# Kernel optimization log

Measured on AMD Instinct MI355X. Metric: run time of the kernel, lower is better.

## Reference

```python
import jax, jax.numpy as jnp
import numpy as np

N_NODES = 50000
N_EDGES = 600000
D = 128

def _linear_params(key, fan_in, fan_out):
    # torch nn.Linear default init: U(-1/sqrt(fan_in), 1/sqrt(fan_in))
    k1, k2 = jax.random.split(key)
    bound = 1.0 / np.sqrt(fan_in)
    W = jax.random.uniform(k1, (fan_in, fan_out), minval=-bound, maxval=bound, dtype=jnp.float32)
    b = jax.random.uniform(k2, (fan_out,), minval=-bound, maxval=bound, dtype=jnp.float32)
    return W, b

def setup_inputs() -> dict:
    key = jax.random.key(0)
    kh, ke, k1, k2, k3, k4 = jax.random.split(key, 6)
    h = jax.random.normal(kh, (N_NODES, D), dtype=jnp.float32)
    edges = jax.random.randint(ke, (N_EDGES, 2), 0, N_NODES, dtype=jnp.int32)
    msg_W1, msg_b1 = _linear_params(k1, 2 * D, D)
    msg_W2, msg_b2 = _linear_params(k2, D, D)
    upd_W1, upd_b1 = _linear_params(k3, 2 * D, D)
    upd_W2, upd_b2 = _linear_params(k4, D, D)
    return {"h": h, "edges": edges,
            "msg_W1": msg_W1, "msg_b1": msg_b1, "msg_W2": msg_W2, "msg_b2": msg_b2,
            "upd_W1": upd_W1, "upd_b1": upd_b1, "upd_W2": upd_W2, "upd_b2": upd_b2}

def reference(h, edges, msg_W1, msg_b1, msg_W2, msg_b2, upd_W1, upd_b1, upd_W2, upd_b2):
    src = edges[:, 0]
    dst = edges[:, 1]
    # message MLP over concatenated [h_src, h_dst] per edge: [E, 2D] -> [E, D]
    pair = jnp.concatenate([h[src], h[dst]], axis=-1)
    msg = jax.nn.relu(pair @ msg_W1 + msg_b1) @ msg_W2 + msg_b2
    # scatter-add aggregate messages onto destination nodes: [N, D]
    agg = jax.ops.segment_sum(msg, dst, num_segments=h.shape[0])
    # update MLP on [h, agg]: [N, 2D] -> [N, D]
    upd_in = jnp.concatenate([h, agg], axis=-1)
    h_new = jax.nn.relu(upd_in @ upd_W1 + upd_b1) @ upd_W2 + upd_b2
    return h + h_new
```

## Files before the change

kernel.cpp:

```cpp
#include <hip/hip_runtime.h>
#include <hip/hip_bf16.h>

#define NN 50000
#define NE 600000
#define TN 64
#define NT ((NN + TN - 1) / TN)
#define CAP 1024

typedef unsigned short u16;
typedef unsigned int u32;
typedef unsigned long long u64;
typedef __attribute__((ext_vector_type(8))) short bf16x8;
typedef __attribute__((ext_vector_type(16))) float f32x16;
typedef __attribute__((ext_vector_type(4))) int int4v;

#define SM_AB   0
#define SM_TT   16384
#define SM_ST   32768
#define SM_S    40960
#define SM_BIAS 49152
#define SMEM_TOTAL 50176

__device__ __forceinline__ void bar_lds() {
    asm volatile("s_waitcnt lgkmcnt(0)" ::: "memory");
    __builtin_amdgcn_s_barrier();
}

__device__ __forceinline__ u16 f2b(float x) {
    __hip_bfloat16 b = __float2bfloat16(x);
    union { __hip_bfloat16 b; u16 u; } c; c.b = b; return c.u;
}
__device__ __forceinline__ int4v zero4() {
    int4v v; v[0]=0; v[1]=0; v[2]=0; v[3]=0; return v;
}
__device__ __forceinline__ f32x16 zero16() {
    f32x16 z;
#pragma unroll
    for (int i = 0; i < 16; ++i) z[i] = 0.f;
    return z;
}
__device__ __forceinline__ int4v cvt8(const float* __restrict__ p) {
    const float4* q = (const float4*)p;
    float4 f0 = q[0], f1 = q[1];
    union { u16 u[8]; int4v v; } r;
    r.u[0]=f2b(f0.x); r.u[1]=f2b(f0.y); r.u[2]=f2b(f0.z); r.u[3]=f2b(f0.w);
    r.u[4]=f2b(f1.x); r.u[5]=f2b(f1.y); r.u[6]=f2b(f1.z); r.u[7]=f2b(f1.w);
    return r.v;
}
__device__ __forceinline__ u64 pack4(float a, float b, float c, float d) {
    union { u16 u[4]; u64 q; } r;
    r.u[0]=f2b(a); r.u[1]=f2b(b); r.u[2]=f2b(c); r.u[3]=f2b(d); return r.q;
}
__device__ __forceinline__ f32x16 mfma16(bf16x8 a, bf16x8 b, f32x16 c) {
    return __builtin_amdgcn_mfma_f32_32x32x16_bf16(a, b, c, 0, 0, 0);
}
__device__ __forceinline__ bf16x8 ld256(const char* base, int row, int c) {
    return *(const bf16x8*)(base + row * 256 + ((c ^ (row & 15)) << 4));
}
__device__ __forceinline__ bf16x8 ld128r(const char* base, int row, int c) {
    return *(const bf16x8*)(base + row * 128 + ((c ^ (row & 7)) << 4));
}

__global__ void prep_kernel(const float* __restrict__ h,
                            const float* __restrict__ W1m, const float* __restrict__ W2m,
                            const float* __restrict__ W1u, const float* __restrict__ W2u,
                            u16* __restrict__ w1tm, u16* __restrict__ w2tm,
                            u16* __restrict__ w1tu, u16* __restrict__ w2tu,
                            u16* __restrict__ hbuf, int do_h)
{
    int tid = blockIdx.x * blockDim.x + threadIdx.x;
    int stride = gridDim.x * blockDim.x;
    for (int i = tid; i < 128 * 256; i += stride) {
        int n = i >> 8, k = i & 255;
        w1tm[i] = f2b(W1m[k * 128 + n]);
        w1tu[i] = f2b(W1u[k * 128 + n]);
    }
    for (int i = tid; i < 128 * 128; i += stride) {
        int n = i >> 7, k = i & 127;
        w2tm[i] = f2b(W2m[k * 128 + n]);
        w2tu[i] = f2b(W2u[k * 128 + n]);
    }
    if (do_h) {
        for (int i = tid; i < NN * 128 / 8; i += stride)
            *(int4v*)(hbuf + (size_t)i * 8) = cvt8(h + (size_t)i * 8);
    }
}

__global__ __launch_bounds__(256) void scatter_kernel(
    const int* __restrict__ edges, u32* __restrict__ elist, int* __restrict__ cursor)
{
    __shared__ int lcnt[NT];
    const int e0 = blockIdx.x * 2048;
    for (int i = threadIdx.x; i < NT; i += 256) lcnt[i] = 0;
    __syncthreads();
#pragma unroll
    for (int k = 0; k < 8; ++k) {
        int e = e0 + k * 256 + threadIdx.x;
        if (e < NE) atomicAdd(&lcnt[edges[2 * e + 1] >> 6], 1);
    }
    __syncthreads();
    for (int i = threadIdx.x; i < NT; i += 256) {
        int cn = lcnt[i];
        if (cn > 0) lcnt[i] = atomicAdd(&cursor[i], cn);
    }
    __syncthreads();
#pragma unroll
    for (int k = 0; k < 8; ++k) {
        int e = e0 + k * 256 + threadIdx.x;
        if (e < NE) {
            int s = edges[2 * e], d = edges[2 * e + 1];
            int bin = d >> 6;
            int pos = atomicAdd(&lcnt[bin], 1);
            if (pos < CAP) elist[(size_t)bin * CAP + pos] = (u32)s | ((u32)(d & 63) << 16);
        }
    }
}

__global__ __launch_bounds__(256, 2) void fused_kernel(
    const float* __restrict__ h, const u16* __restrict__ hb, int use_hb,
    const u32* __restrict__ elist, const int* __restrict__ cursor,
    const u16* __restrict__ w1m, const u16* __restrict__ w2m,
    const u16* __restrict__ w1u, const u16* __restrict__ w2u,
    const float* __restrict__ b1m, const float* __restrict__ b2m,
    const float* __restrict__ b1u, const float* __restrict__ b2u,
    float* __restrict__ outp)
{
    extern __shared__ char sm[];
    char* ab   = sm + SM_AB;
    char* ttr  = sm + SM_TT;
    char* Stb  = sm + SM_ST;
    char* Sb   = sm + SM_S;
    char* bias = sm + SM_BIAS;
    char* htu  = sm + SM_ST;

    const int tid  = threadIdx.x;
    const int lane = tid & 63;
    const int wid  = tid >> 6;
    const int l31  = lane & 31;
    const int kg   = lane >> 5;
    const int nrow  = wid * 32 + l31;
    const int ecol0 = l31;
    const int ecol1 = 32 + l31;

    const int bin = blockIdx.x;
    const int n0  = bin * TN;
    int size = cursor[bin]; if (size > CAP) size = CAP;
    const u32* el = elist + (size_t)bin * CAP;
    const int nchunk = (size + 63) >> 6;

    bf16x8 w1f[8], w2f[8];
#pragma unroll
    for (int kk = 0; kk < 8; ++kk) {
        w1f[kk] = *(const bf16x8*)(w1m + nrow * 256 + (kk * 2 + kg) * 8);
        w2f[kk] = *(const bf16x8*)(w2m + nrow * 128 + (kk * 2 + kg) * 8);
    }
    const float b2ms = b2m[nrow];

    for (int i = tid; i < 1024; i += 256) {
        int row = i >> 4, c = i & 15;
        int node = n0 + row;
        int4v v = zero4();
        if (node < NN) {
            if (use_hb) v = *(const int4v*)(hb + (size_t)node * 128 + c * 8);
            else        v = cvt8(h + (size_t)node * 128 + c * 8);
        }
        *(int4v*)(ttr + row * 256 + ((c ^ (row & 15)) << 4)) = v;
    }
    if (tid < 32)      *(float4*)(bias + tid * 16)          = ((const float4*)b1m)[tid];
    else if (tid < 64) *(float4*)(bias + 512 + (tid-32)*16) = ((const float4*)b1u)[tid - 32];
    {
        char* z = sm + SM_ST + tid * 64;
        *(int4v*)z = zero4(); *(int4v*)(z + 16) = zero4();
        *(int4v*)(z + 32) = zero4(); *(int4v*)(z + 48) = zero4();
    }

    auto put_St = [&](u32 rec, int cb2, u16 val) {
        if (cb2 + lane < size) {
            int d = (int)((rec >> 16) & 63);
            *(u16*)(Stb + lane * 128 + (((d >> 3) ^ (lane & 7)) << 4) + (d & 7) * 2) = val;
        }
    };
    auto put_S = [&](u32 rec, int cb2, u16 val) {
        if (cb2 + lane < size) {
            int d = (int)((rec >> 16) & 63);
            *(u16*)(Sb + d * 128 + (((lane >> 3) ^ (d & 7)) << 4) + (lane & 7) * 2) = val;
        }
    };

    const int s_row0 = tid >> 4, s_cc = tid & 15;
    auto stage_load = [&](u32 dle_c, int cb2, int4v* v) {
#pragma unroll
        for (int u = 0; u < 4; ++u) {
            int row = s_row0 + 16 * u;
            int s = ((int)__shfl((int)dle_c, row, 64)) & 0xFFFF;
            v[u] = zero4();
            if (cb2 + row < size)
                v[u] = use_hb ? *(const int4v*)(hb + (size_t)s * 128 + s_cc * 8)
                              : cvt8(h + (size_t)s * 128 + s_cc * 8);
        }
    };
    auto stage_write = [&](const int4v* v) {
#pragma unroll
        for (int u = 0; u < 4; ++u) {
            int row = s_row0 + 16 * u;
            *(int4v*)(ab + row * 256 + ((s_cc ^ (row & 15)) << 4)) = v[u];
        }
    };

    auto mkfrags = [&](const f32x16& cc, bf16x8& lo, bf16x8& hi) {
        u32 u0,u1,u2,u3,u4,u5,u6,u7;
        {
            float a0=cc[0]+b2ms, a1=cc[1]+b2ms, a2=cc[2]+b2ms, a3=cc[3]+b2ms;
            float a4=cc[4]+b2ms, a5=cc[5]+b2ms, a6=cc[6]+b2ms, a7=cc[7]+b2ms;
            float a8=cc[8]+b2ms, a9=cc[9]+b2ms, aA=cc[10]+b2ms, aB=cc[11]+b2ms;
            float aC=cc[12]+b2ms, aD=cc[13]+b2ms, aE=cc[14]+b2ms, aF=cc[15]+b2ms;
            asm("v_cvt_pk_bf16_f32 %0, %1, %2" : "=v"(u0) : "v"(a0), "v"(a1));
            asm("v_cvt_pk_bf16_f32 %0, %1, %2" : "=v"(u1) : "v"(a2), "v"(a3));
            asm("v_cvt_pk_bf16_f32 %0, %1, %2" : "=v"(u2) : "v"(a4), "v"(a5));
            asm("v_cvt_pk_bf16_f32 %0, %1, %2" : "=v"(u3) : "v"(a6), "v"(a7));
            asm("v_cvt_pk_bf16_f32 %0, %1, %2" : "=v"(u4) : "v"(a8), "v"(a9));
            asm("v_cvt_pk_bf16_f32 %0, %1, %2" : "=v"(u5) : "v"(aA), "v"(aB));
            asm("v_cvt_pk_bf16_f32 %0, %1, %2" : "=v"(u6) : "v"(aC), "v"(aD));
            asm("v_cvt_pk_bf16_f32 %0, %1, %2" : "=v"(u7) : "v"(aE), "v"(aF));
        }
        asm volatile("v_permlane32_swap_b32 %0, %1" : "+v"(u0), "+v"(u2));
        asm volatile("v_permlane32_swap_b32 %0, %1" : "+v"(u1), "+v"(u3));
        asm volatile("v_permlane32_swap_b32 %0, %1" : "+v"(u4), "+v"(u6));
        asm volatile("v_permlane32_swap_b32 %0, %1" : "+v"(u5), "+v"(u7));
        union { u32 w[4]; bf16x8 v; } A, B;
        A.w[0]=u0; A.w[1]=u1; A.w[2]=u2; A.w[3]=u3;
        B.w[0]=u4; B.w[1]=u5; B.w[2]=u6; B.w[3]=u7;
        lo = A.v; hi = B.v;
    };

    u32 dle = (lane < size) ? el[lane] : 0u;
    if (nchunk > 0) {
        int4v v[4];
        stage_load(dle, 0, v);
        stage_write(v);
    }
    __syncthreads();

    f32x16 t0 = zero16(), t1 = zero16();
    {
        __builtin_amdgcn_s_setprio(1);
#pragma unroll
        for (int kk = 0; kk < 8; ++kk) {
            bf16x8 wtf = *(const bf16x8*)(w1m + nrow * 256 + (16 + kk * 2 + kg) * 8);
            int ch = kk * 2 + kg;
            t0 = mfma16(wtf, ld256(ttr, ecol0, ch), t0);
            t1 = mfma16(wtf, ld256(ttr, ecol1, ch), t1);
        }
        __builtin_amdgcn_s_setprio(0);
    }
    if (wid == 0) { put_St(dle, 0, 0x3F80); put_S(dle, 0, 0x3F80); }
    bar_lds();

#pragma unroll
    for (int r = 0; r < 16; ++r) {
        int n1 = wid * 32 + (r & 3) + 8 * (r >> 2) + 4 * kg;
        *(u16*)(ttr + n1 * 128 + (((ecol0 >> 3) ^ (n1 & 7)) << 4) + (ecol0 & 7) * 2) = f2b(t0[r]);
        *(u16*)(ttr + n1 * 128 + (((ecol1 >> 3) ^ (n1 & 7)) << 4) + (ecol1 & 7) * 2) = f2b(t1[r]);
    }
    bar_lds();

    f32x16 aggT0 = zero16(), aggT1 = zero16();
    u32 dle_prev = 0;
    for (int c = 0; c < nchunk; ++c) {
        const int cb = c << 6;
        const bool havepf = (c + 1 < nchunk);

        u32 dle_next = (havepf && (cb + 64 + lane < size)) ? el[cb + 64 + lane] : 0u;

        f32x16 mm0 = zero16(), mm1 = zero16();
        __builtin_amdgcn_s_setprio(1);
#pragma unroll
        for (int kk = 0; kk < 4; ++kk) {
            int ch = kk * 2 + kg;
            bf16x8 ttf = ld128r(ttr, nrow, ch);
            mm0 = mfma16(ttf, ld128r(Stb, ecol0, ch), mm0);
            mm1 = mfma16(ttf, ld128r(Stb, ecol1, ch), mm1);
        }
#pragma unroll
        for (int kk = 0; kk < 8; ++kk) {
            int ch = kk * 2 + kg;
            mm0 = mfma16(w1f[kk], ld256(ab, ecol0, ch), mm0);
            mm1 = mfma16(w1f[kk], ld256(ab, ecol1, ch), mm1);
        }
        __builtin_amdgcn_s_setprio(0);
        bar_lds();

        int4v v[4];
        if (havepf) stage_load(dle_next, cb + 64, v);
#pragma unroll
        for (int rq = 0; rq < 4; ++rq) {
            float4 bq = *(const float4*)(bias + (wid * 32 + 8 * rq + 4 * kg) * 4);
            int cch = wid * 4 + rq;
            u64 q0 = pack4(fmaxf(mm0[4 * rq + 0] + bq.x, 0.f),
                           fmaxf(mm0[4 * rq + 1] + bq.y, 0.f),
                           fmaxf(mm0[4 * rq + 2] + bq.z, 0.f),
                           fmaxf(mm0[4 * rq + 3] + bq.w, 0.f));
            u64 q1 = pack4(fmaxf(mm1[4 * rq + 0] + bq.x, 0.f),
                           fmaxf(mm1[4 * rq + 1] + bq.y, 0.f),
                           fmaxf(mm1[4 * rq + 2] + bq.z, 0.f),
                           fmaxf(mm1[4 * rq + 3] + bq.w, 0.f));
            *(u64*)(ab + ecol0 * 256 + ((cch ^ (ecol0 & 15)) << 4) + 8 * kg) = q0;
            *(u64*)(ab + ecol1 * 256 + ((cch ^ (ecol1 & 15)) << 4) + 8 * kg) = q1;
        }
        if (wid == 0) {
            if (c > 0) put_S(dle_prev, cb - 64, 0);
            put_St(dle, cb, 0);
            asm volatile("s_waitcnt lgkmcnt(0)" ::: "memory");
            put_St(dle_next, cb + 64, 0x3F80);
            put_S(dle, cb, 0x3F80);
        }
        bar_lds();

        {
            f32x16 c20 = zero16(), c21 = zero16();
            __builtin_amdgcn_s_setprio(1);
#pragma unroll
            for (int kk = 0; kk < 8; ++kk) {
                int ch = kk * 2 + kg;
                c20 = mfma16(ld256(ab, ecol0, ch), w2f[kk], c20);
                c21 = mfma16(ld256(ab, ecol1, ch), w2f[kk], c21);
            }
            __builtin_amdgcn_s_setprio(0);
            bf16x8 fA, fB, fC, fD;
            mkfrags(c20, fA, fB);
            mkfrags(c21, fC, fD);
            __builtin_amdgcn_s_setprio(1);
            aggT0 = mfma16(fA, ld128r(Sb, ecol0, 0 + kg), aggT0);
            aggT1 = mfma16(fA, ld128r(Sb, ecol1, 0 + kg), aggT1);
            aggT0 = mfma16(fB, ld128r(Sb, ecol0, 2 + kg), aggT0);
            aggT1 = mfma16(fB, ld128r(Sb, ecol1, 2 + kg), aggT1);
            aggT0 = mfma16(fC, ld128r(Sb, ecol0, 4 + kg), aggT0);
            aggT1 = mfma16(fC, ld128r(Sb, ecol1, 4 + kg), aggT1);
            aggT0 = mfma16(fD, ld128r(Sb, ecol0, 6 + kg), aggT0);
            aggT1 = mfma16(fD, ld128r(Sb, ecol1, 6 + kg), aggT1);
            __builtin_amdgcn_s_setprio(0);
        }
        bar_lds();

        if (havepf) stage_write(v);
        bar_lds();
        dle_prev = dle;
        dle = dle_next;
    }

#pragma unroll
    for (int rq = 0; rq < 4; ++rq) {
        int cch = wid * 4 + rq;
        u64 q0 = pack4(aggT0[4 * rq + 0], aggT0[4 * rq + 1], aggT0[4 * rq + 2], aggT0[4 * rq + 3]);
        u64 q1 = pack4(aggT1[4 * rq + 0], aggT1[4 * rq + 1], aggT1[4 * rq + 2], aggT1[4 * rq + 3]);
        *(u64*)(ab + ecol0 * 256 + ((cch ^ (ecol0 & 15)) << 4) + 8 * kg) = q0;
        *(u64*)(ab + ecol1 * 256 + ((cch ^ (ecol1 & 15)) << 4) + 8 * kg) = q1;
    }
    for (int i = tid; i < 1024; i += 256) {
        int row = i >> 4, c = i & 15;
        int node = n0 + row;
        int4v v = zero4();
        if (node < NN) {
            if (use_hb) v = *(const int4v*)(hb + (size_t)node * 128 + c * 8);
            else        v = cvt8(h + (size_t)node * 128 + c * 8);
        }
        *(int4v*)(htu + row * 256 + ((c ^ (row & 15)) << 4)) = v;
    }
    bar_lds();

    {
        f32x16 au0 = zero16(), au1 = zero16();
        {
            bf16x8 wa[8];
#pragma unroll
            for (int kk = 0; kk < 8; ++kk)
                wa[kk] = *(const bf16x8*)(w1u + nrow * 256 + (kk * 2 + kg) * 8);
            __builtin_amdgcn_s_setprio(1);
#pragma unroll
            for (int kk = 0; kk < 8; ++kk) {
                int ch = kk * 2 + kg;
                au0 = mfma16(wa[kk], ld256(htu, ecol0, ch), au0);
                au1 = mfma16(wa[kk], ld256(htu, ecol1, ch), au1);
            }
            __builtin_amdgcn_s_setprio(0);
        }
        {
            bf16x8 wbf[8];
#pragma unroll
            for (int kk = 0; kk < 8; ++kk)
                wbf[kk] = *(const bf16x8*)(w1u + nrow * 256 + ((8 + kk) * 2 + kg) * 8);
            __builtin_amdgcn_s_setprio(1);
#pragma unroll
            for (int kk = 0; kk < 8; ++kk) {
                int ch = kk * 2 + kg;
                au0 = mfma16(wbf[kk], ld256(ab, ecol0, ch), au0);
                au1 = mfma16(wbf[kk], ld256(ab, ecol1, ch), au1);
            }
            __builtin_amdgcn_s_setprio(0);
        }
        bar_lds();
#pragma unroll
        for (int rq = 0; rq < 4; ++rq) {
            float4 bq = *(const float4*)(bias + 512 + (wid * 32 + 8 * rq + 4 * kg) * 4);
            int cch = wid * 4 + rq;
            u64 q0 = pack4(fmaxf(au0[4 * rq + 0] + bq.x, 0.f),
                           fmaxf(au0[4 * rq + 1] + bq.y, 0.f),
                           fmaxf(au0[4 * rq + 2] + bq.z, 0.f),
                           fmaxf(au0[4 * rq + 3] + bq.w, 0.f));
            u64 q1 = pack4(fmaxf(au1[4 * rq + 0] + bq.x, 0.f),
                           fmaxf(au1[4 * rq + 1] + bq.y, 0.f),
                           fmaxf(au1[4 * rq + 2] + bq.z, 0.f),
                           fmaxf(au1[4 * rq + 3] + bq.w, 0.f));
            *(u64*)(ttr + ecol0 * 256 + ((cch ^ (ecol0 & 15)) << 4) + 8 * kg) = q0;
            *(u64*)(ttr + ecol1 * 256 + ((cch ^ (ecol1 & 15)) << 4) + 8 * kg) = q1;
        }
    }
    bar_lds();

    {
        bf16x8 wc[8];
#pragma unroll
        for (int kk = 0; kk < 8; ++kk)
            wc[kk] = *(const bf16x8*)(w2u + nrow * 128 + (kk * 2 + kg) * 8);
        const float b2us = b2u[nrow];
        f32x16 cu0 = zero16(), cu1 = zero16();
        __builtin_amdgcn_s_setprio(1);
#pragma unroll
        for (int kk = 0; kk < 8; ++kk) {
            int ch = kk * 2 + kg;
            cu0 = mfma16(ld256(ttr, ecol0, ch), wc[kk], cu0);
            cu1 = mfma16(ld256(ttr, ecol1, ch), wc[kk], cu1);
        }
        __builtin_amdgcn_s_setprio(0);
#pragma unroll
        for (int r = 0; r < 16; ++r) {
            int rmap = (r & 3) + 8 * (r >> 2) + 4 * kg;
            int ng0 = n0 + rmap;
            int ng1 = n0 + 32 + rmap;
            if (ng0 < NN) {
                size_t o = (size_t)ng0 * 128 + nrow;
                outp[o] = cu0[r] + b2us + h[o];
            }
            if (ng1 < NN) {
                size_t o = (size_t)ng1 * 128 + nrow;
                outp[o] = cu1[r] + b2us + h[o];
            }
        }
    }
}

extern "C" void kernel_launch(void* const* d_in, const int* in_sizes, int n_in,
                              void* d_out, int out_size, void* d_ws, size_t ws_size,
                              hipStream_t stream) {
    const float* h   = (const float*)d_in[0];
    const int* edges = (const int*)d_in[1];
    const float* W1m = (const float*)d_in[2];
    const float* b1m = (const float*)d_in[3];
    const float* W2m = (const float*)d_in[4];
    const float* b2m = (const float*)d_in[5];
    const float* W1u = (const float*)d_in[6];
    const float* b1u = (const float*)d_in[7];
    const float* W2u = (const float*)d_in[8];
    const float* b2u = (const float*)d_in[9];
    float* out = (float*)d_out;

    char* ws = (char*)d_ws;
    u16* w1tm  = (u16*)(ws + 0);
    u16* w2tm  = (u16*)(ws + 65536);
    u16* w1tu  = (u16*)(ws + 98304);
    u16* w2tu  = (u16*)(ws + 163840);
    int* curs  = (int*)(ws + 196608);
    u32* elist = (u32*)(ws + 200704);
    u16* hb    = (u16*)(ws + 3403776);
    int use_hb = (ws_size >= 3403776ull + (size_t)NN * 128 * 2) ? 1 : 0;

    (void)hipFuncSetAttribute((const void*)fused_kernel,
                              hipFuncAttributeMaxDynamicSharedMemorySize, SMEM_TOTAL);

    hipMemsetAsync(curs, 0, NT * sizeof(int), stream);
    prep_kernel<<<512, 256, 0, stream>>>(h, W1m, W2m, W1u, W2u,
                                         w1tm, w2tm, w1tu, w2tu, hb, use_hb);
    scatter_kernel<<<(NE + 2047) / 2048, 256, 0, stream>>>(edges, elist, curs);
    fused_kernel<<<NT, 256, SMEM_TOTAL, stream>>>(h, hb, use_hb, elist, curs,
                                                  w1tm, w2tm, w1tu, w2tu,
                                                  b1m, b2m, b1u, b2u, out);
}
```

Before: 152.3 us.

## Double-buffer gathered edge tiles in LDS and issue gathers earlier

Splits the single 16KB edge staging buffer into two ping-pong buffers, so each chunk's gathered h rows are written into the alternate buffer. The global gather for the next chunk now starts at the top of the iteration, before the first MFMA phase, and the edge-list index is fetched two chunks ahead. This drops one LDS barrier per chunk and gives the gather more latency to hide. In exchange, LDS use rises to about 66KB per block, and the prefetched vectors stay live across the MFMA loops, which raises register pressure under the two-blocks-per-CU launch bound.

```diff
diff --git a/kernel.cpp b/kernel.cpp
--- a/kernel.cpp
+++ b/kernel.cpp
@@ -14,12 +14,13 @@
 typedef __attribute__((ext_vector_type(16))) float f32x16;
 typedef __attribute__((ext_vector_type(4))) int int4v;
 
-#define SM_AB   0
-#define SM_TT   16384
-#define SM_ST   32768
-#define SM_S    40960
-#define SM_BIAS 49152
-#define SMEM_TOTAL 50176
+#define SM_AB0  0
+#define SM_AB1  16384
+#define SM_TT   32768
+#define SM_ST   49152
+#define SM_S    57344
+#define SM_BIAS 65536
+#define SMEM_TOTAL 66560
 
 __device__ __forceinline__ void bar_lds() {
     asm volatile("s_waitcnt lgkmcnt(0)" ::: "memory");
@@ -126,7 +127,8 @@
     float* __restrict__ outp)
 {
     extern __shared__ char sm[];
-    char* ab   = sm + SM_AB;
+    char* ab0  = sm + SM_AB0;
+    char* ab1  = sm + SM_AB1;
     char* ttr  = sm + SM_TT;
     char* Stb  = sm + SM_ST;
     char* Sb   = sm + SM_S;
@@ -199,11 +201,11 @@
                               : cvt8(h + (size_t)s * 128 + s_cc * 8);
         }
     };
-    auto stage_write = [&](const int4v* v) {
+    auto stage_write = [&](char* base, const int4v* v) {
 #pragma unroll
         for (int u = 0; u < 4; ++u) {
             int row = s_row0 + 16 * u;
-            *(int4v*)(ab + row * 256 + ((s_cc ^ (row & 15)) << 4)) = v[u];
+            *(int4v*)(base + row * 256 + ((s_cc ^ (row & 15)) << 4)) = v[u];
         }
     };
 
@@ -233,11 +235,12 @@
         lo = A.v; hi = B.v;
     };
 
-    u32 dle = (lane < size) ? el[lane] : 0u;
+    u32 dle    = (lane < size) ? el[lane] : 0u;
+    u32 dle_nx = (64 + lane < size) ? el[64 + lane] : 0u;
     if (nchunk > 0) {
         int4v v[4];
         stage_load(dle, 0, v);
-        stage_write(v);
+        stage_write(ab0, v);
     }
     __syncthreads();
 
@@ -268,9 +271,13 @@
     u32 dle_prev = 0;
     for (int c = 0; c < nchunk; ++c) {
         const int cb = c << 6;
-        const bool havepf = (c + 1 < nchunk);
-
-        u32 dle_next = (havepf && (cb + 64 + lane < size)) ? el[cb + 64 + lane] : 0u;
+        const bool havepf  = (c + 1 < nchunk);
+        char* prc = (c & 1) ? ab1 : ab0;
+        char* prn = (c & 1) ? ab0 : ab1;
+
+        int4v v[4];
+        if (havepf) stage_load(dle_nx, cb + 64, v);
+        u32 dle_nx2 = (c + 2 < nchunk && cb + 128 + lane < size) ? el[cb + 128 + lane] : 0u;
 
         f32x16 mm0 = zero16(), mm1 = zero16();
         __builtin_amdgcn_s_setprio(1);
@@ -284,14 +291,12 @@
 #pragma unroll
         for (int kk = 0; kk < 8; ++kk) {
             int ch = kk * 2 + kg;
-            mm0 = mfma16(w1f[kk], ld256(ab, ecol0, ch), mm0);
-            mm1 = mfma16(w1f[kk], ld256(ab, ecol1, ch), mm1);
+            mm0 = mfma16(w1f[kk], ld256(prc, ecol0, ch), mm0);
+            mm1 = mfma16(w1f[kk], ld256(prc, ecol1, ch), mm1);
         }
         __builtin_amdgcn_s_setprio(0);
         bar_lds();
 
-        int4v v[4];
-        if (havepf) stage_load(dle_next, cb + 64, v);
 #pragma unroll
         for (int rq = 0; rq < 4; ++rq) {
             float4 bq = *(const float4*)(bias + (wid * 32 + 8 * rq + 4 * kg) * 4);
@@ -304,14 +309,15 @@
                            fmaxf(mm1[4 * rq + 1] + bq.y, 0.f),
                            fmaxf(mm1[4 * rq + 2] + bq.z, 0.f),
                            fmaxf(mm1[4 * rq + 3] + bq.w, 0.f));
-            *(u64*)(ab + ecol0 * 256 + ((cch ^ (ecol0 & 15)) << 4) + 8 * kg) = q0;
-            *(u64*)(ab + ecol1 * 256 + ((cch ^ (ecol1 & 15)) << 4) + 8 * kg) = q1;
-        }
+            *(u64*)(prc + ecol0 * 256 + ((cch ^ (ecol0 & 15)) << 4) + 8 * kg) = q0;
+            *(u64*)(prc + ecol1 * 256 + ((cch ^ (ecol1 & 15)) << 4) + 8 * kg) = q1;
+        }
+        if (havepf) stage_write(prn, v);
         if (wid == 0) {
             if (c > 0) put_S(dle_prev, cb - 64, 0);
             put_St(dle, cb, 0);
             asm volatile("s_waitcnt lgkmcnt(0)" ::: "memory");
-            put_St(dle_next, cb + 64, 0x3F80);
+            put_St(dle_nx, cb + 64, 0x3F80);
             put_S(dle, cb, 0x3F80);
         }
         bar_lds();
@@ -322,8 +328,8 @@
 #pragma unroll
             for (int kk = 0; kk < 8; ++kk) {
                 int ch = kk * 2 + kg;
-                c20 = mfma16(ld256(ab, ecol0, ch), w2f[kk], c20);
-                c21 = mfma16(ld256(ab, ecol1, ch), w2f[kk], c21);
+                c20 = mfma16(ld256(prc, ecol0, ch), w2f[kk], c20);
+                c21 = mfma16(ld256(prc, ecol1, ch), w2f[kk], c21);
             }
             __builtin_amdgcn_s_setprio(0);
             bf16x8 fA, fB, fC, fD;
@@ -342,10 +348,9 @@
         }
         bar_lds();
 
-        if (havepf) stage_write(v);
-        bar_lds();
         dle_prev = dle;
-        dle = dle_next;
+        dle = dle_nx;
+        dle_nx = dle_nx2;
     }
 
 #pragma unroll
@@ -353,8 +358,8 @@
         int cch = wid * 4 + rq;
         u64 q0 = pack4(aggT0[4 * rq + 0], aggT0[4 * rq + 1], aggT0[4 * rq + 2], aggT0[4 * rq + 3]);
         u64 q1 = pack4(aggT1[4 * rq + 0], aggT1[4 * rq + 1], aggT1[4 * rq + 2], aggT1[4 * rq + 3]);
-        *(u64*)(ab + ecol0 * 256 + ((cch ^ (ecol0 & 15)) << 4) + 8 * kg) = q0;
-        *(u64*)(ab + ecol1 * 256 + ((cch ^ (ecol1 & 15)) << 4) + 8 * kg) = q1;
+        *(u64*)(ab0 + ecol0 * 256 + ((cch ^ (ecol0 & 15)) << 4) + 8 * kg) = q0;
+        *(u64*)(ab0 + ecol1 * 256 + ((cch ^ (ecol1 & 15)) << 4) + 8 * kg) = q1;
     }
     for (int i = tid; i < 1024; i += 256) {
         int row = i >> 4, c = i & 15;
@@ -393,8 +398,8 @@
 #pragma unroll
             for (int kk = 0; kk < 8; ++kk) {
                 int ch = kk * 2 + kg;
-                au0 = mfma16(wbf[kk], ld256(ab, ecol0, ch), au0);
-                au1 = mfma16(wbf[kk], ld256(ab, ecol1, ch), au1);
+                au0 = mfma16(wbf[kk], ld256(ab0, ecol0, ch), au0);
+                au1 = mfma16(wbf[kk], ld256(ab0, ecol1, ch), au1);
             }
             __builtin_amdgcn_s_setprio(0);
         }
```

Measured after the change: 154.2 us. No clear change (+1.2%).
